# Performance work log

Measured on AMD Instinct MI355X. Metric: run time of the kernel, lower is better.

## Reference

```python
import jax, jax.numpy as jnp
import numpy as np

N_NODES = 50000
N_EDGES = 800000


def _sage_mean(x, src, dst, w, W_self, W_neigh, b, n_nodes):
    # DGL SAGEConv('mean') with edge_weight: messages m_e = w_e * h[src_e],
    # h_neigh[v] = sum_{e->v} m_e / in_degree(v)  (zero if no in-edges),
    # out = h @ W_self + h_neigh @ W_neigh + b
    msg = x[src] * w[:, None]                                   # [E, d]
    s = jax.ops.segment_sum(msg, dst, num_segments=n_nodes)     # [N, d]
    deg = jax.ops.segment_sum(jnp.ones_like(w), dst, num_segments=n_nodes)
    h_neigh = s / jnp.clip(deg, 1.0)[:, None]
    return x @ W_self + h_neigh @ W_neigh + b


def setup_inputs() -> dict:
    key = jax.random.key(0)
    ks = jax.random.split(key, 12)
    d_in, d_h = 64, 256
    inp = {
        'features': jax.random.normal(ks[0], (N_NODES, d_in), dtype=jnp.float32),
        'edge_src': jax.random.randint(ks[1], (N_EDGES,), 0, N_NODES, dtype=jnp.int32),
        'edge_dst': jax.random.randint(ks[2], (N_EDGES,), 0, N_NODES, dtype=jnp.int32),
        'edge_weights': jax.random.uniform(ks[3], (N_EDGES,), dtype=jnp.float32),
        'W1_self': jax.random.normal(ks[4], (d_in, d_h), dtype=jnp.float32) * (1.0 / np.sqrt(d_in)),
        'W1_neigh': jax.random.normal(ks[5], (d_in, d_h), dtype=jnp.float32) * (1.0 / np.sqrt(d_in)),
        'b1': jnp.zeros((d_h,), dtype=jnp.float32),
        'W2_self': jax.random.normal(ks[6], (d_h, 128), dtype=jnp.float32) * (1.0 / np.sqrt(d_h)),
        'W2_neigh': jax.random.normal(ks[7], (d_h, 128), dtype=jnp.float32) * (1.0 / np.sqrt(d_h)),
        'b2': jnp.zeros((128,), dtype=jnp.float32),
        'Wl1': jax.random.normal(ks[8], (128, 64), dtype=jnp.float32) * (1.0 / np.sqrt(128)),
        'bl1': jnp.zeros((64,), dtype=jnp.float32),
        'Wl2': jax.random.normal(ks[9], (64, 32), dtype=jnp.float32) * (1.0 / np.sqrt(64)),
        'bl2': jnp.zeros((32,), dtype=jnp.float32),
        'Wl3': jax.random.normal(ks[10], (32, 10), dtype=jnp.float32) * (1.0 / np.sqrt(32)),
        'bl3': jnp.zeros((10,), dtype=jnp.float32),
    }
    return inp


def reference(features, edge_src, edge_dst, edge_weights,
              W1_self, W1_neigh, b1, W2_self, W2_neigh, b2,
              Wl1, bl1, Wl2, bl2, Wl3, bl3):
    n = features.shape[0]
    x = features.reshape(n, -1)  # flatten (already 2D)
    x = jax.nn.relu(_sage_mean(x, edge_src, edge_dst, edge_weights,
                               W1_self, W1_neigh, b1, n))
    # conv2 is applied twice on identical inputs in the original; results are equal
    embeddings = _sage_mean(x, edge_src, edge_dst, edge_weights,
                            W2_self, W2_neigh, b2, n)
    h = jax.nn.relu(embeddings @ Wl1 + bl1)
    h = jax.nn.relu(h @ Wl2 + bl2)
    out = h @ Wl3 + bl3
    return (out, embeddings)
```

## Files before the change

kernel.cpp:

```cpp
#include <hip/hip_runtime.h>
#include <hip/hip_bf16.h>

#define N_NODES 50000
#define N_EDGES 800000
#define MT_TILES 3125
#define PR_TILES 1563

#define NBLK_SORT 200
#define CHUNK_SORT 4000
#define NBKT 196

typedef __attribute__((ext_vector_type(8))) short frag_ab;
typedef __attribute__((ext_vector_type(4))) float frag_cd;

static __device__ __forceinline__ unsigned short f2b(float f) {
    union { float f; unsigned u; } v; v.f = f;
    unsigned r = v.u + 0x7fffu + ((v.u >> 16) & 1u);
    return (unsigned short)(r >> 16);
}
static __device__ __forceinline__ float b2f(unsigned short b) {
    union { float f; unsigned u; } v; v.u = ((unsigned)b) << 16;
    return v.f;
}
static __device__ __forceinline__ float blo(unsigned p) { return b2f((unsigned short)(p & 0xffffu)); }
static __device__ __forceinline__ float bhi(unsigned p) { return b2f((unsigned short)(p >> 16)); }

static __device__ __forceinline__ unsigned short packBK_elem(const float* __restrict__ Wa,
                                                             const float* __restrict__ Wb,
                                                             int Ka, int N, int idx) {
    int j = idx & 7;
    int lane = (idx >> 3) & 63;
    int rest = idx >> 9;
    int ntiles = N >> 4;
    int nt = rest % ntiles;
    int kt = rest / ntiles;
    int kk = kt * 32 + (lane >> 4) * 8 + j;
    int nn = nt * 16 + (lane & 15);
    float v = (kk < Ka) ? Wa[kk * N + nn] : Wb[(kk - Ka) * N + nn];
    return f2b(v);
}
static __device__ __forceinline__ unsigned short packBN_elem(const float* __restrict__ Wa,
                                                             const float* __restrict__ Wb,
                                                             int Na, int N, int idx) {
    int j = idx & 7;
    int lane = (idx >> 3) & 63;
    int rest = idx >> 9;
    int ntiles = N >> 4;
    int nt = rest % ntiles;
    int kt = rest / ntiles;
    int kk = kt * 32 + (lane >> 4) * 8 + j;
    int nn = nt * 16 + (lane & 15);
    float v = (nn < Na) ? Wa[kk * Na + nn] : Wb[kk * (N - Na) + (nn - Na)];
    return f2b(v);
}

#define PREP_S0 800000
#define PREP_S1 (PREP_S0 + 32768)
#define PREP_S2 (PREP_S1 + 65536)
#define PREP_S3 (PREP_S2 + 8192)
#define PREP_S4 (PREP_S3 + 2048)
#define PREP_BLKS 3549

__global__ __launch_bounds__(256) void prep_p1_kernel(const float4* __restrict__ x4,
                                                      ushort4* __restrict__ xb4,
                                                      const float* __restrict__ W1s,
                                                      const float* __restrict__ W1n,
                                                      const float* __restrict__ W2s,
                                                      const float* __restrict__ W2n,
                                                      const float* __restrict__ Wl1,
                                                      const float* __restrict__ Wl2,
                                                      unsigned short* __restrict__ B1p,
                                                      unsigned short* __restrict__ B2p,
                                                      unsigned short* __restrict__ Bl1p,
                                                      unsigned short* __restrict__ Bl2p,
                                                      const int* __restrict__ dst,
                                                      int* __restrict__ G) {
    __shared__ int h[256];
    int bid = blockIdx.x;
    int t = threadIdx.x;
    if (bid >= PREP_BLKS) {
        int blk = bid - PREP_BLKS;
        h[t] = 0;
        __syncthreads();
        int base = blk * CHUNK_SORT;
        for (int i = t; i < CHUNK_SORT; i += 256)
            atomicAdd(&h[dst[base + i] >> 8], 1);
        __syncthreads();
        G[blk * 256 + t] = h[t];
        return;
    }
    int idx = bid * 256 + t;
    if (idx < PREP_S0) {
        float4 v = x4[idx];
        ushort4 o;
        o.x = f2b(v.x); o.y = f2b(v.y); o.z = f2b(v.z); o.w = f2b(v.w);
        xb4[idx] = o;
    } else if (idx < PREP_S1) {
        int i = idx - PREP_S0;
        B1p[i] = packBK_elem(W1s, W1n, 64, 256, i);
    } else if (idx < PREP_S2) {
        int i = idx - PREP_S1;
        B2p[i] = packBN_elem(W2s, W2n, 128, 256, i);
    } else if (idx < PREP_S3) {
        int i = idx - PREP_S2;
        Bl1p[i] = packBK_elem(Wl1, Wl1, 128, 64, i);
    } else {
        int i = idx - PREP_S3;
        Bl2p[i] = packBK_elem(Wl2, Wl2, 64, 32, i);
    }
}


__global__ __launch_bounds__(256) void p2a_scan(int* __restrict__ G,
                                                int* __restrict__ colsum) {
    __shared__ int sc[256];
    int b = blockIdx.x;
    int t = threadIdx.x;
    int v = (t < NBLK_SORT) ? G[t * 256 + b] : 0;
    sc[t] = v;
    __syncthreads();
    for (int off = 1; off < 256; off <<= 1) {
        int add = (t >= off) ? sc[t - off] : 0;
        __syncthreads();
        sc[t] += add;
        __syncthreads();
    }
    if (t < NBLK_SORT) G[t * 256 + b] = sc[t] - v;
    if (t == 255) colsum[b] = sc[255];
}

__global__ __launch_bounds__(256) void p2b_scan(const int* __restrict__ colsum,
                                                int* __restrict__ bucket_off,
                                                int* __restrict__ row_off) {
    __shared__ int sc[256];
    int t = threadIdx.x;
    int v = colsum[t];
    sc[t] = v;
    __syncthreads();
    for (int off = 1; off < 256; off <<= 1) {
        int add = (t >= off) ? sc[t - off] : 0;
        __syncthreads();
        sc[t] += add;
        __syncthreads();
    }
    bucket_off[t] = sc[t] - v;
    if (t == 255) row_off[N_NODES] = sc[255];
}

__global__ __launch_bounds__(256) void p3_scatter(const int* __restrict__ src,
                                                  const int* __restrict__ dst,
                                                  const float* __restrict__ w,
                                                  const int* __restrict__ G,
                                                  const int* __restrict__ bucket_off,
                                                  int* __restrict__ bdst,
                                                  int2* __restrict__ bsedge) {
    __shared__ int cur[256];
    int t = threadIdx.x;
    cur[t] = G[blockIdx.x * 256 + t] + bucket_off[t];
    __syncthreads();
    int base = blockIdx.x * CHUNK_SORT;
    for (int i = t; i < CHUNK_SORT; i += 256) {
        int e = base + i;
        int d = dst[e];
        int pos = atomicAdd(&cur[d >> 8], 1);
        bdst[pos] = d;
        bsedge[pos] = make_int2(src[e], __float_as_int(w[e]));
    }
}

__global__ __launch_bounds__(256) void p4_sort(const int* __restrict__ bucket_off,
                                               const int* __restrict__ bdst,
                                               const int2* __restrict__ bsedge,
                                               int* __restrict__ row_off,
                                               float* __restrict__ inv_deg,
                                               int2* __restrict__ sedge) {
    __shared__ int lcnt[256];
    __shared__ int lcur[256];
    __shared__ int sc[256];
    int t = threadIdx.x;
    int b = blockIdx.x;
    int e0 = bucket_off[b], e1 = bucket_off[b + 1];
    int d0 = b << 8;
    lcnt[t] = 0;
    __syncthreads();
    for (int e = e0 + t; e < e1; e += 256)
        atomicAdd(&lcnt[bdst[e] - d0], 1);
    __syncthreads();
    int v = lcnt[t];
    sc[t] = v;
    __syncthreads();
    for (int off = 1; off < 256; off <<= 1) {
        int add = (t >= off) ? sc[t - off] : 0;
        __syncthreads();
        sc[t] += add;
        __syncthreads();
    }
    int loff = e0 + sc[t] - v;
    lcur[t] = loff;
    int d = d0 + t;
    if (d < N_NODES) {
        row_off[d] = loff;
        inv_deg[d] = 1.0f / (float)(v > 0 ? v : 1);
    }
    __syncthreads();
    for (int e = e0 + t; e < e1; e += 256) {
        int dd = bdst[e];
        int2 sv = bsedge[e];
        int pos = atomicAdd(&lcur[dd - d0], 1);
        sedge[pos] = sv;
    }
}


__global__ __launch_bounds__(256) void agg64_kernel(const uint2* __restrict__ xb2,
                                                    const int* __restrict__ row_off,
                                                    const int2* __restrict__ sedge,
                                                    const float* __restrict__ inv_deg,
                                                    uint2* __restrict__ hn1b2) {
    int tid = threadIdx.x;
    int lane = tid & 63;
    int qr = lane >> 4;
    int l15 = lane & 15;
    int n = blockIdx.x * 4 + (tid >> 6);
    if (n >= N_NODES) return;
    int e0 = row_off[n], e1 = row_off[n + 1];
    float a0 = 0.f, a1 = 0.f, a2 = 0.f, a3 = 0.f;
    int e = e0;
    for (; e + 16 <= e1; e += 16) {
        int2 m0 = sedge[e + qr];
        int2 m1 = sedge[e + 4 + qr];
        int2 m2 = sedge[e + 8 + qr];
        int2 m3 = sedge[e + 12 + qr];
        uint2 p0 = xb2[m0.x * 16 + l15];
        uint2 p1 = xb2[m1.x * 16 + l15];
        uint2 p2 = xb2[m2.x * 16 + l15];
        uint2 p3 = xb2[m3.x * 16 + l15];
        float w0 = __int_as_float(m0.y), w1 = __int_as_float(m1.y);
        float w2 = __int_as_float(m2.y), w3 = __int_as_float(m3.y);
        a0 += w0 * blo(p0.x) + w1 * blo(p1.x) + w2 * blo(p2.x) + w3 * blo(p3.x);
        a1 += w0 * bhi(p0.x) + w1 * bhi(p1.x) + w2 * bhi(p2.x) + w3 * bhi(p3.x);
        a2 += w0 * blo(p0.y) + w1 * blo(p1.y) + w2 * blo(p2.y) + w3 * blo(p3.y);
        a3 += w0 * bhi(p0.y) + w1 * bhi(p1.y) + w2 * bhi(p2.y) + w3 * bhi(p3.y);
    }
    for (; e < e1; e += 4) {
        int ee = e + qr;
        if (ee < e1) {
            int2 m = sedge[ee];
            uint2 p = xb2[m.x * 16 + l15];
            float w = __int_as_float(m.y);
            a0 += w * blo(p.x); a1 += w * bhi(p.x);
            a2 += w * blo(p.y); a3 += w * bhi(p.y);
        }
    }
    a0 += __shfl_xor(a0, 16, 64); a1 += __shfl_xor(a1, 16, 64);
    a2 += __shfl_xor(a2, 16, 64); a3 += __shfl_xor(a3, 16, 64);
    a0 += __shfl_xor(a0, 32, 64); a1 += __shfl_xor(a1, 32, 64);
    a2 += __shfl_xor(a2, 32, 64); a3 += __shfl_xor(a3, 32, 64);
    if (qr == 0) {
        float id = inv_deg[n];
        uint2 o;
        o.x = (unsigned)f2b(a0 * id) | ((unsigned)f2b(a1 * id) << 16);
        o.y = (unsigned)f2b(a2 * id) | ((unsigned)f2b(a3 * id) << 16);
        hn1b2[n * 16 + l15] = o;
    }
}

__global__ __launch_bounds__(256) void agg128_kernel(const uint2* __restrict__ zb2,
                                                     const int* __restrict__ row_off,
                                                     const int2* __restrict__ sedge,
                                                     const float* __restrict__ inv_deg,
                                                     float* __restrict__ emb,
                                                     uint2* __restrict__ embb2) {
    int tid = threadIdx.x;
    int lane = tid & 63;
    int hf = lane >> 5;
    int l31 = lane & 31;
    int n = blockIdx.x * 4 + (tid >> 6);
    if (n >= N_NODES) return;
    int e0 = row_off[n], e1 = row_off[n + 1];
    float a0 = 0.f, a1 = 0.f, a2 = 0.f, a3 = 0.f;
    int e = e0;
    for (; e + 16 <= e1; e += 16) {
        int2 m0 = sedge[e + hf];
        int2 m1 = sedge[e + 2 + hf];
        int2 m2 = sedge[e + 4 + hf];
        int2 m3 = sedge[e + 6 + hf];
        int2 m4 = sedge[e + 8 + hf];
        int2 m5 = sedge[e + 10 + hf];
        int2 m6 = sedge[e + 12 + hf];
        int2 m7 = sedge[e + 14 + hf];
        uint2 p0 = zb2[m0.x * 32 + l31];
        uint2 p1 = zb2[m1.x * 32 + l31];
        uint2 p2 = zb2[m2.x * 32 + l31];
        uint2 p3 = zb2[m3.x * 32 + l31];
        uint2 p4 = zb2[m4.x * 32 + l31];
        uint2 p5 = zb2[m5.x * 32 + l31];
        uint2 p6 = zb2[m6.x * 32 + l31];
        uint2 p7 = zb2[m7.x * 32 + l31];
        float w0 = __int_as_float(m0.y), w1 = __int_as_float(m1.y);
        float w2 = __int_as_float(m2.y), w3 = __int_as_float(m3.y);
        float w4 = __int_as_float(m4.y), w5 = __int_as_float(m5.y);
        float w6 = __int_as_float(m6.y), w7 = __int_as_float(m7.y);
        a0 += w0 * blo(p0.x) + w1 * blo(p1.x) + w2 * blo(p2.x) + w3 * blo(p3.x)
            + w4 * blo(p4.x) + w5 * blo(p5.x) + w6 * blo(p6.x) + w7 * blo(p7.x);
        a1 += w0 * bhi(p0.x) + w1 * bhi(p1.x) + w2 * bhi(p2.x) + w3 * bhi(p3.x)
            + w4 * bhi(p4.x) + w5 * bhi(p5.x) + w6 * bhi(p6.x) + w7 * bhi(p7.x);
        a2 += w0 * blo(p0.y) + w1 * blo(p1.y) + w2 * blo(p2.y) + w3 * blo(p3.y)
            + w4 * blo(p4.y) + w5 * blo(p5.y) + w6 * blo(p6.y) + w7 * blo(p7.y);
        a3 += w0 * bhi(p0.y) + w1 * bhi(p1.y) + w2 * bhi(p2.y) + w3 * bhi(p3.y)
            + w4 * bhi(p4.y) + w5 * bhi(p5.y) + w6 * bhi(p6.y) + w7 * bhi(p7.y);
    }
    for (; e < e1; e += 2) {
        int ee = e + hf;
        if (ee < e1) {
            int2 m = sedge[ee];
            uint2 p = zb2[m.x * 32 + l31];
            float w = __int_as_float(m.y);
            a0 += w * blo(p.x); a1 += w * bhi(p.x);
            a2 += w * blo(p.y); a3 += w * bhi(p.y);
        }
    }
    a0 += __shfl_xor(a0, 32, 64); a1 += __shfl_xor(a1, 32, 64);
    a2 += __shfl_xor(a2, 32, 64); a3 += __shfl_xor(a3, 32, 64);
    if (hf == 0) {
        float id = inv_deg[n];
        float4 self = ((const float4*)emb)[n * 32 + l31];
        float v0 = self.x + a0 * id;
        float v1 = self.y + a1 * id;
        float v2 = self.z + a2 * id;
        float v3 = self.w + a3 * id;
        ((float4*)emb)[n * 32 + l31] = make_float4(v0, v1, v2, v3);
        uint2 o;
        o.x = (unsigned)f2b(v0) | ((unsigned)f2b(v1) << 16);
        o.y = (unsigned)f2b(v2) | ((unsigned)f2b(v3) << 16);
        embb2[n * 32 + l31] = o;
    }
}


__global__ __launch_bounds__(256) void gemm1_mfma(const unsigned short* __restrict__ xb,
                                                  const unsigned short* __restrict__ hn1b,
                                                  const unsigned short* __restrict__ Bp,
                                                  const float* __restrict__ b1,
                                                  unsigned short* __restrict__ x1b) {
    __shared__ __align__(16) unsigned short sB[8192];
    int tid = threadIdx.x;
    int lane = tid & 63;
    int wv = tid >> 6;
    int mt = blockIdx.x * 4 + wv;
    if (mt >= MT_TILES) mt = MT_TILES - 1;
    int q = lane >> 4;
    int rl = lane & 15;
    int row = mt * 16 + rl;
    frag_ab a[4];
    a[0] = *(const frag_ab*)(xb + row * 64 + q * 8);
    a[1] = *(const frag_ab*)(xb + row * 64 + q * 8 + 32);
    a[2] = *(const frag_ab*)(hn1b + row * 64 + q * 8);
    a[3] = *(const frag_ab*)(hn1b + row * 64 + q * 8 + 32);
    frag_cd acc[16];
    #pragma unroll
    for (int nt = 0; nt < 16; nt++) acc[nt] = (frag_cd){0.f, 0.f, 0.f, 0.f};
    #pragma unroll
    for (int kt = 0; kt < 4; kt++) {
        __syncthreads();
        #pragma unroll
        for (int i = 0; i < 4; i++) {
            int idx = i * 256 + tid;
            ((float4*)sB)[idx] = ((const float4*)(Bp + kt * 8192))[idx];
        }
        __syncthreads();
        #pragma unroll
        for (int nt = 0; nt < 16; nt++) {
            frag_ab b = *(const frag_ab*)(sB + (nt * 64 + lane) * 8);
            acc[nt] = __builtin_amdgcn_mfma_f32_16x16x32_bf16(a[kt], b, acc[nt], 0, 0, 0);
        }
    }
    int r0 = mt * 16;
    #pragma unroll
    for (int nt = 0; nt < 16; nt++) {
        int c = nt * 16 + rl;
        float bias = b1[c];
        #pragma unroll
        for (int i = 0; i < 4; i++) {
            int r = r0 + q * 4 + i;
            float v = acc[nt][i] + bias;
            v = v > 0.f ? v : 0.f;
            x1b[r * 256 + c] = f2b(v);
        }
    }
}

__global__ __launch_bounds__(256) void gemm2_mfma(const unsigned short* __restrict__ x1b,
                                                  const unsigned short* __restrict__ Bp,
                                                  const float* __restrict__ b2,
                                                  float* __restrict__ emb,
                                                  unsigned short* __restrict__ zb) {
    __shared__ __align__(16) unsigned short sB[8192];
    int tid = threadIdx.x;
    int lane = tid & 63;
    int wv = tid >> 6;
    int mt = blockIdx.x * 4 + wv;
    if (mt >= MT_TILES) mt = MT_TILES - 1;
    int q = lane >> 4;
    int rl = lane & 15;
    int row = mt * 16 + rl;
    const unsigned short* arow = x1b + row * 256 + q * 8;
    frag_ab a[8];
    #pragma unroll
    for (int kt = 0; kt < 8; kt++) a[kt] = *(const frag_ab*)(arow + kt * 32);
    frag_cd acc[16];
    #pragma unroll
    for (int nt = 0; nt < 16; nt++) acc[nt] = (frag_cd){0.f, 0.f, 0.f, 0.f};
    #pragma unroll
    for (int kt = 0; kt < 8; kt++) {
        __syncthreads();
        #pragma unroll
        for (int i = 0; i < 4; i++) {
            int idx = i * 256 + tid;
            ((float4*)sB)[idx] = ((const float4*)(Bp + kt * 8192))[idx];
        }
        __syncthreads();
        #pragma unroll
        for (int nt = 0; nt < 16; nt++) {
            frag_ab b = *(const frag_ab*)(sB + (nt * 64 + lane) * 8);
            acc[nt] = __builtin_amdgcn_mfma_f32_16x16x32_bf16(a[kt], b, acc[nt], 0, 0, 0);
        }
    }
    int r0 = mt * 16;
    #pragma unroll
    for (int nt = 0; nt < 8; nt++) {
        int c = nt * 16 + rl;
        float bias = b2[c];
        #pragma unroll
        for (int i = 0; i < 4; i++) {
            int r = r0 + q * 4 + i;
            emb[r * 128 + c] = acc[nt][i] + bias;
        }
    }
    #pragma unroll
    for (int nt = 8; nt < 16; nt++) {
        int c = (nt - 8) * 16 + rl;
        #pragma unroll
        for (int i = 0; i < 4; i++) {
            int r = r0 + q * 4 + i;
            zb[r * 128 + c] = f2b(acc[nt][i]);
        }
    }
}

__global__ __launch_bounds__(256) void mlp1_mfma(const unsigned short* __restrict__ embb,
                                                 const unsigned short* __restrict__ Bp,
                                                 const float* __restrict__ bl1,
                                                 unsigned short* __restrict__ h64b) {
    int tid = threadIdx.x;
    int lane = tid & 63;
    int wv = tid >> 6;
    int pr = blockIdx.x * 4 + wv;
    if (pr >= PR_TILES) pr = PR_TILES - 1;
    int mt0 = pr * 2;
    int mt1 = mt0 + 1; if (mt1 >= MT_TILES) mt1 = MT_TILES - 1;
    int q = lane >> 4;
    int rl = lane & 15;
    const unsigned short* a0row = embb + (mt0 * 16 + rl) * 128 + q * 8;
    const unsigned short* a1row = embb + (mt1 * 16 + rl) * 128 + q * 8;
    const frag_ab* bp = (const frag_ab*)Bp;
    frag_cd acc0[4], acc1[4];
    #pragma unroll
    for (int nt = 0; nt < 4; nt++) {
        acc0[nt] = (frag_cd){0.f, 0.f, 0.f, 0.f};
        acc1[nt] = (frag_cd){0.f, 0.f, 0.f, 0.f};
    }
    #pragma unroll
    for (int kt = 0; kt < 4; kt++) {
        frag_ab a0 = *(const frag_ab*)(a0row + kt * 32);
        frag_ab a1 = *(const frag_ab*)(a1row + kt * 32);
        #pragma unroll
        for (int nt = 0; nt < 4; nt++) {
            frag_ab b = bp[(kt * 4 + nt) * 64 + lane];
            acc0[nt] = __builtin_amdgcn_mfma_f32_16x16x32_bf16(a0, b, acc0[nt], 0, 0, 0);
            acc1[nt] = __builtin_amdgcn_mfma_f32_16x16x32_bf16(a1, b, acc1[nt], 0, 0, 0);
        }
    }
    int r0a = mt0 * 16 + q * 4, r0b = mt1 * 16 + q * 4;
    #pragma unroll
    for (int nt = 0; nt < 4; nt++) {
        int c = nt * 16 + rl;
        float bias = bl1[c];
        #pragma unroll
        for (int i = 0; i < 4; i++) {
            float v0 = acc0[nt][i] + bias;
            float v1 = acc1[nt][i] + bias;
            h64b[(r0a + i) * 64 + c] = f2b(v0 > 0.f ? v0 : 0.f);
            h64b[(r0b + i) * 64 + c] = f2b(v1 > 0.f ? v1 : 0.f);
        }
    }
}

__global__ __launch_bounds__(256) void mlp23_mfma(const unsigned short* __restrict__ h64b,
                                                  const unsigned short* __restrict__ Bp,
                                                  const float* __restrict__ bl2,
                                                  const float* __restrict__ Wl3,
                                                  const float* __restrict__ bl3,
                                                  float* __restrict__ out) {
    __shared__ float hs[64][33];
    int tid = threadIdx.x;
    int lane = tid & 63;
    int wv = tid >> 6;
    int mt = blockIdx.x * 4 + wv;
    if (mt >= MT_TILES) mt = MT_TILES - 1;
    int q = lane >> 4;
    int rl = lane & 15;
    const unsigned short* arow = h64b + (mt * 16 + rl) * 64 + q * 8;
    const frag_ab* bp = (const frag_ab*)Bp;
    frag_cd acc[2];
    #pragma unroll
    for (int nt = 0; nt < 2; nt++) acc[nt] = (frag_cd){0.f, 0.f, 0.f, 0.f};
    #pragma unroll
    for (int kt = 0; kt < 2; kt++) {
        frag_ab a = *(const frag_ab*)(arow + kt * 32);
        #pragma unroll
        for (int nt = 0; nt < 2; nt++) {
            frag_ab b = bp[(kt * 2 + nt) * 64 + lane];
            acc[nt] = __builtin_amdgcn_mfma_f32_16x16x32_bf16(a, b, acc[nt], 0, 0, 0);
        }
    }
    #pragma unroll
    for (int nt = 0; nt < 2; nt++) {
        int c = nt * 16 + rl;
        float bias = bl2[c];
        #pragma unroll
        for (int i = 0; i < 4; i++) {
            int lr = wv * 16 + q * 4 + i;
            float v = acc[nt][i] + bias;
            hs[lr][c] = v > 0.f ? v : 0.f;
        }
    }
    __syncthreads();
    int base = blockIdx.x * 64;
    for (int idx = tid; idx < 640; idx += 256) {
        int lr = idx / 10;
        int j = idx - lr * 10;
        int n = base + lr;
        if (n < N_NODES) {
            float a = bl3[j];
            #pragma unroll
            for (int k = 0; k < 32; k++) a += hs[lr][k] * Wl3[k * 10 + j];
            out[n * 10 + j] = a;
        }
    }
}


extern "C" void kernel_launch(void* const* d_in, const int* in_sizes, int n_in,
                              void* d_out, int out_size, void* d_ws, size_t ws_size,
                              hipStream_t stream) {
    const float* x   = (const float*)d_in[0];
    const int* esrc  = (const int*)d_in[1];
    const int* edst  = (const int*)d_in[2];
    const float* ew  = (const float*)d_in[3];
    const float* W1s = (const float*)d_in[4];
    const float* W1n = (const float*)d_in[5];
    const float* b1  = (const float*)d_in[6];
    const float* W2s = (const float*)d_in[7];
    const float* W2n = (const float*)d_in[8];
    const float* b2  = (const float*)d_in[9];
    const float* Wl1 = (const float*)d_in[10];
    const float* bl1 = (const float*)d_in[11];
    const float* Wl2 = (const float*)d_in[12];
    const float* bl2 = (const float*)d_in[13];
    const float* Wl3 = (const float*)d_in[14];
    const float* bl3 = (const float*)d_in[15];

    float* out = (float*)d_out;
    float* emb = out + 500000;

    char* ws = (char*)d_ws;
    size_t off = 0;
    auto alloc = [&](size_t bytes) -> void* {
        void* p = ws + off;
        off = (off + bytes + 255) & ~(size_t)255;
        return p;
    };
    int*   row_off = (int*)alloc((size_t)(N_NODES + 1) * 4);
    float* inv_deg = (float*)alloc((size_t)N_NODES * 4);
    int*   G       = (int*)alloc((size_t)NBLK_SORT * 256 * 4);
    int*   colsum  = (int*)alloc(256 * 4);
    int*   bkt_off = (int*)alloc(257 * 4);
    int*   bdst    = (int*)alloc((size_t)N_EDGES * 4);
    int2*  bsedge  = (int2*)alloc((size_t)N_EDGES * 8);
    int2*  sedge   = (int2*)alloc((size_t)N_EDGES * 8);
    unsigned short* xb   = (unsigned short*)alloc((size_t)N_NODES * 64 * 2);
    unsigned short* hn1b = (unsigned short*)alloc((size_t)N_NODES * 64 * 2);
    unsigned short* x1b  = (unsigned short*)alloc((size_t)N_NODES * 256 * 2);
    unsigned short* zb   = (unsigned short*)alloc((size_t)N_NODES * 128 * 2);
    unsigned short* embb = (unsigned short*)alloc((size_t)N_NODES * 128 * 2);
    unsigned short* h64b = (unsigned short*)alloc((size_t)N_NODES * 64 * 2);
    unsigned short* B1p  = (unsigned short*)alloc(128 * 256 * 2);
    unsigned short* B2p  = (unsigned short*)alloc(256 * 256 * 2);
    unsigned short* Bl1p = (unsigned short*)alloc(128 * 64 * 2);
    unsigned short* Bl2p = (unsigned short*)alloc(64 * 32 * 2);

    prep_p1_kernel<<<PREP_BLKS + NBLK_SORT, 256, 0, stream>>>(
        (const float4*)x, (ushort4*)xb, W1s, W1n, W2s, W2n, Wl1, Wl2,
        B1p, B2p, Bl1p, Bl2p, edst, G);

    p2a_scan<<<256, 256, 0, stream>>>(G, colsum);
    p2b_scan<<<1, 256, 0, stream>>>(colsum, bkt_off, row_off);
    p3_scatter<<<NBLK_SORT, 256, 0, stream>>>(esrc, edst, ew, G, bkt_off, bdst, bsedge);
    p4_sort<<<NBKT, 256, 0, stream>>>(bkt_off, bdst, bsedge, row_off, inv_deg, sedge);

    const int PBLK = (PR_TILES + 3) / 4;
    const int GBLK = (MT_TILES + 3) / 4;
    const int ABLK = (N_NODES + 3) / 4;

    agg64_kernel<<<ABLK, 256, 0, stream>>>((const uint2*)xb, row_off, sedge,
                                           inv_deg, (uint2*)hn1b);
    gemm1_mfma<<<GBLK, 256, 0, stream>>>(xb, hn1b, B1p, b1, x1b);

    gemm2_mfma<<<GBLK, 256, 0, stream>>>(x1b, B2p, b2, emb, zb);
    agg128_kernel<<<ABLK, 256, 0, stream>>>((const uint2*)zb, row_off, sedge,
                                            inv_deg, emb, (uint2*)embb);

    mlp1_mfma<<<PBLK, 256, 0, stream>>>(embb, Bl1p, bl1, h64b);
    mlp23_mfma<<<GBLK, 256, 0, stream>>>(h64b, Bl2p, bl2, Wl3, bl3, out);
}
```

Baseline: 279.9 us.

## Split aggregation kernels into feature slices and store self term as bf16

Both aggregation kernels now launch several grids of node groups, each block handling one 32-feature slice. Each lane gathers one 32-bit bf16 pair per edge instead of 8 bytes, so the gathered feature working set per pass is smaller and should cache better. gemm2 now writes its self-projection plus bias in bf16 into a combined 256-wide buffer rather than an fp32 emb array. agg128 reads that self term and writes the final fp32 emb and its bf16 copy. The cost is reading the edge lists and row offsets several times over, and rounding the self term to bf16 before it reaches the embeddings.

```diff
diff --git a/kernel.cpp b/kernel.cpp
--- a/kernel.cpp
+++ b/kernel.cpp
@@ -9,6 +9,7 @@
 #define NBLK_SORT 200
 #define CHUNK_SORT 4000
 #define NBKT 196
+#define AGG_G 12500
 
 typedef __attribute__((ext_vector_type(8))) short frag_ab;
 typedef __attribute__((ext_vector_type(4))) float frag_cd;
@@ -212,128 +213,131 @@
 }
 
 
-__global__ __launch_bounds__(256) void agg64_kernel(const uint2* __restrict__ xb2,
+__global__ __launch_bounds__(256) void agg64_kernel(const unsigned* __restrict__ xb32,
                                                     const int* __restrict__ row_off,
                                                     const int2* __restrict__ sedge,
                                                     const float* __restrict__ inv_deg,
-                                                    uint2* __restrict__ hn1b2) {
+                                                    unsigned* __restrict__ hn1b32) {
+    int bi = blockIdx.x;
+    int s = bi / AGG_G;
+    int g = bi - s * AGG_G;
     int tid = threadIdx.x;
     int lane = tid & 63;
     int qr = lane >> 4;
     int l15 = lane & 15;
-    int n = blockIdx.x * 4 + (tid >> 6);
-    if (n >= N_NODES) return;
+    int n = g * 4 + (tid >> 6);
+    int xoff = s * 16 + l15;
     int e0 = row_off[n], e1 = row_off[n + 1];
-    float a0 = 0.f, a1 = 0.f, a2 = 0.f, a3 = 0.f;
+    float a0 = 0.f, a1 = 0.f;
     int e = e0;
-    for (; e + 16 <= e1; e += 16) {
+    for (; e + 32 <= e1; e += 32) {
         int2 m0 = sedge[e + qr];
         int2 m1 = sedge[e + 4 + qr];
         int2 m2 = sedge[e + 8 + qr];
         int2 m3 = sedge[e + 12 + qr];
-        uint2 p0 = xb2[m0.x * 16 + l15];
-        uint2 p1 = xb2[m1.x * 16 + l15];
-        uint2 p2 = xb2[m2.x * 16 + l15];
-        uint2 p3 = xb2[m3.x * 16 + l15];
+        int2 m4 = sedge[e + 16 + qr];
+        int2 m5 = sedge[e + 20 + qr];
+        int2 m6 = sedge[e + 24 + qr];
+        int2 m7 = sedge[e + 28 + qr];
+        unsigned p0 = xb32[m0.x * 32 + xoff];
+        unsigned p1 = xb32[m1.x * 32 + xoff];
+        unsigned p2 = xb32[m2.x * 32 + xoff];
+        unsigned p3 = xb32[m3.x * 32 + xoff];
+        unsigned p4 = xb32[m4.x * 32 + xoff];
+        unsigned p5 = xb32[m5.x * 32 + xoff];
+        unsigned p6 = xb32[m6.x * 32 + xoff];
+        unsigned p7 = xb32[m7.x * 32 + xoff];
         float w0 = __int_as_float(m0.y), w1 = __int_as_float(m1.y);
         float w2 = __int_as_float(m2.y), w3 = __int_as_float(m3.y);
-        a0 += w0 * blo(p0.x) + w1 * blo(p1.x) + w2 * blo(p2.x) + w3 * blo(p3.x);
-        a1 += w0 * bhi(p0.x) + w1 * bhi(p1.x) + w2 * bhi(p2.x) + w3 * bhi(p3.x);
-        a2 += w0 * blo(p0.y) + w1 * blo(p1.y) + w2 * blo(p2.y) + w3 * blo(p3.y);
-        a3 += w0 * bhi(p0.y) + w1 * bhi(p1.y) + w2 * bhi(p2.y) + w3 * bhi(p3.y);
+        float w4 = __int_as_float(m4.y), w5 = __int_as_float(m5.y);
+        float w6 = __int_as_float(m6.y), w7 = __int_as_float(m7.y);
+        a0 += w0 * blo(p0) + w1 * blo(p1) + w2 * blo(p2) + w3 * blo(p3)
+            + w4 * blo(p4) + w5 * blo(p5) + w6 * blo(p6) + w7 * blo(p7);
+        a1 += w0 * bhi(p0) + w1 * bhi(p1) + w2 * bhi(p2) + w3 * bhi(p3)
+            + w4 * bhi(p4) + w5 * bhi(p5) + w6 * bhi(p6) + w7 * bhi(p7);
     }
     for (; e < e1; e += 4) {
         int ee = e + qr;
         if (ee < e1) {
             int2 m = sedge[ee];
-            uint2 p = xb2[m.x * 16 + l15];
+            unsigned p = xb32[m.x * 32 + xoff];
             float w = __int_as_float(m.y);
-            a0 += w * blo(p.x); a1 += w * bhi(p.x);
-            a2 += w * blo(p.y); a3 += w * bhi(p.y);
+            a0 += w * blo(p);
+            a1 += w * bhi(p);
         }
     }
     a0 += __shfl_xor(a0, 16, 64); a1 += __shfl_xor(a1, 16, 64);
-    a2 += __shfl_xor(a2, 16, 64); a3 += __shfl_xor(a3, 16, 64);
     a0 += __shfl_xor(a0, 32, 64); a1 += __shfl_xor(a1, 32, 64);
-    a2 += __shfl_xor(a2, 32, 64); a3 += __shfl_xor(a3, 32, 64);
     if (qr == 0) {
         float id = inv_deg[n];
-        uint2 o;
-        o.x = (unsigned)f2b(a0 * id) | ((unsigned)f2b(a1 * id) << 16);
-        o.y = (unsigned)f2b(a2 * id) | ((unsigned)f2b(a3 * id) << 16);
-        hn1b2[n * 16 + l15] = o;
-    }
-}
-
-__global__ __launch_bounds__(256) void agg128_kernel(const uint2* __restrict__ zb2,
+        hn1b32[n * 32 + xoff] = (unsigned)f2b(a0 * id) | ((unsigned)f2b(a1 * id) << 16);
+    }
+}
+
+__global__ __launch_bounds__(256) void agg128_kernel(const unsigned* __restrict__ sz32,
                                                      const int* __restrict__ row_off,
                                                      const int2* __restrict__ sedge,
                                                      const float* __restrict__ inv_deg,
                                                      float* __restrict__ emb,
-                                                     uint2* __restrict__ embb2) {
+                                                     unsigned* __restrict__ embb32) {
+    int bi = blockIdx.x;
+    int s = bi / AGG_G;
+    int g = bi - s * AGG_G;
     int tid = threadIdx.x;
     int lane = tid & 63;
-    int hf = lane >> 5;
-    int l31 = lane & 31;
-    int n = blockIdx.x * 4 + (tid >> 6);
-    if (n >= N_NODES) return;
+    int qr = lane >> 4;
+    int l15 = lane & 15;
+    int n = g * 4 + (tid >> 6);
+    int soff = s * 16 + l15;
+    int zoff = 64 + soff;
     int e0 = row_off[n], e1 = row_off[n + 1];
-    float a0 = 0.f, a1 = 0.f, a2 = 0.f, a3 = 0.f;
+    float a0 = 0.f, a1 = 0.f;
     int e = e0;
-    for (; e + 16 <= e1; e += 16) {
-        int2 m0 = sedge[e + hf];
-        int2 m1 = sedge[e + 2 + hf];
-        int2 m2 = sedge[e + 4 + hf];
-        int2 m3 = sedge[e + 6 + hf];
-        int2 m4 = sedge[e + 8 + hf];
-        int2 m5 = sedge[e + 10 + hf];
-        int2 m6 = sedge[e + 12 + hf];
-        int2 m7 = sedge[e + 14 + hf];
-        uint2 p0 = zb2[m0.x * 32 + l31];
-        uint2 p1 = zb2[m1.x * 32 + l31];
-        uint2 p2 = zb2[m2.x * 32 + l31];
-        uint2 p3 = zb2[m3.x * 32 + l31];
-        uint2 p4 = zb2[m4.x * 32 + l31];
-        uint2 p5 = zb2[m5.x * 32 + l31];
-        uint2 p6 = zb2[m6.x * 32 + l31];
-        uint2 p7 = zb2[m7.x * 32 + l31];
+    for (; e + 32 <= e1; e += 32) {
+        int2 m0 = sedge[e + qr];
+        int2 m1 = sedge[e + 4 + qr];
+        int2 m2 = sedge[e + 8 + qr];
+        int2 m3 = sedge[e + 12 + qr];
+        int2 m4 = sedge[e + 16 + qr];
+        int2 m5 = sedge[e + 20 + qr];
+        int2 m6 = sedge[e + 24 + qr];
+        int2 m7 = sedge[e + 28 + qr];
+        unsigned p0 = sz32[m0.x * 128 + zoff];
+        unsigned p1 = sz32[m1.x * 128 + zoff];
+        unsigned p2 = sz32[m2.x * 128 + zoff];
+        unsigned p3 = sz32[m3.x * 128 + zoff];
+        unsigned p4 = sz32[m4.x * 128 + zoff];
+        unsigned p5 = sz32[m5.x * 128 + zoff];
+        unsigned p6 = sz32[m6.x * 128 + zoff];
+        unsigned p7 = sz32[m7.x * 128 + zoff];
         float w0 = __int_as_float(m0.y), w1 = __int_as_float(m1.y);
         float w2 = __int_as_float(m2.y), w3 = __int_as_float(m3.y);
         float w4 = __int_as_float(m4.y), w5 = __int_as_float(m5.y);
         float w6 = __int_as_float(m6.y), w7 = __int_as_float(m7.y);
-        a0 += w0 * blo(p0.x) + w1 * blo(p1.x) + w2 * blo(p2.x) + w3 * blo(p3.x)
-            + w4 * blo(p4.x) + w5 * blo(p5.x) + w6 * blo(p6.x) + w7 * blo(p7.x);
-        a1 += w0 * bhi(p0.x) + w1 * bhi(p1.x) + w2 * bhi(p2.x) + w3 * bhi(p3.x)
-            + w4 * bhi(p4.x) + w5 * bhi(p5.x) + w6 * bhi(p6.x) + w7 * bhi(p7.x);
-        a2 += w0 * blo(p0.y) + w1 * blo(p1.y) + w2 * blo(p2.y) + w3 * blo(p3.y)
-            + w4 * blo(p4.y) + w5 * blo(p5.y) + w6 * blo(p6.y) + w7 * blo(p7.y);
-        a3 += w0 * bhi(p0.y) + w1 * bhi(p1.y) + w2 * bhi(p2.y) + w3 * bhi(p3.y)
-            + w4 * bhi(p4.y) + w5 * bhi(p5.y) + w6 * bhi(p6.y) + w7 * bhi(p7.y);
-    }
-    for (; e < e1; e += 2) {
-        int ee = e + hf;
+        a0 += w0 * blo(p0) + w1 * blo(p1) + w2 * blo(p2) + w3 * blo(p3)
+            + w4 * blo(p4) + w5 * blo(p5) + w6 * blo(p6) + w7 * blo(p7);
+        a1 += w0 * bhi(p0) + w1 * bhi(p1) + w2 * bhi(p2) + w3 * bhi(p3)
+            + w4 * bhi(p4) + w5 * bhi(p5) + w6 * bhi(p6) + w7 * bhi(p7);
+    }
+    for (; e < e1; e += 4) {
+        int ee = e + qr;
         if (ee < e1) {
             int2 m = sedge[ee];
-            uint2 p = zb2[m.x * 32 + l31];
+            unsigned p = sz32[m.x * 128 + zoff];
             float w = __int_as_float(m.y);
-            a0 += w * blo(p.x); a1 += w * bhi(p.x);
-            a2 += w * blo(p.y); a3 += w * bhi(p.y);
-        }
-    }
+            a0 += w * blo(p);
+            a1 += w * bhi(p);
+        }
+    }
+    a0 += __shfl_xor(a0, 16, 64); a1 += __shfl_xor(a1, 16, 64);
     a0 += __shfl_xor(a0, 32, 64); a1 += __shfl_xor(a1, 32, 64);
-    a2 += __shfl_xor(a2, 32, 64); a3 += __shfl_xor(a3, 32, 64);
-    if (hf == 0) {
+    if (qr == 0) {
         float id = inv_deg[n];
-        float4 self = ((const float4*)emb)[n * 32 + l31];
-        float v0 = self.x + a0 * id;
-        float v1 = self.y + a1 * id;
-        float v2 = self.z + a2 * id;
-        float v3 = self.w + a3 * id;
-        ((float4*)emb)[n * 32 + l31] = make_float4(v0, v1, v2, v3);
-        uint2 o;
-        o.x = (unsigned)f2b(v0) | ((unsigned)f2b(v1) << 16);
-        o.y = (unsigned)f2b(v2) | ((unsigned)f2b(v3) << 16);
-        embb2[n * 32 + l31] = o;
+        unsigned sp = sz32[n * 128 + soff];
+        float vx = blo(sp) + a0 * id;
+        float vy = bhi(sp) + a1 * id;
+        ((float2*)emb)[n * 64 + soff] = make_float2(vx, vy);
+        embb32[n * 64 + soff] = (unsigned)f2b(vx) | ((unsigned)f2b(vy) << 16);
     }
 }
 
@@ -393,8 +397,7 @@
 __global__ __launch_bounds__(256) void gemm2_mfma(const unsigned short* __restrict__ x1b,
                                                   const unsigned short* __restrict__ Bp,
                                                   const float* __restrict__ b2,
-                                                  float* __restrict__ emb,
-                                                  unsigned short* __restrict__ zb) {
+                                                  unsigned short* __restrict__ sz) {
     __shared__ __align__(16) unsigned short sB[8192];
     int tid = threadIdx.x;
     int lane = tid & 63;
@@ -428,22 +431,13 @@
     }
     int r0 = mt * 16;
     #pragma unroll
-    for (int nt = 0; nt < 8; nt++) {
+    for (int nt = 0; nt < 16; nt++) {
         int c = nt * 16 + rl;
-        float bias = b2[c];
+        float bias = (nt < 8) ? b2[c] : 0.f;
         #pragma unroll
         for (int i = 0; i < 4; i++) {
             int r = r0 + q * 4 + i;
-            emb[r * 128 + c] = acc[nt][i] + bias;
-        }
-    }
-    #pragma unroll
-    for (int nt = 8; nt < 16; nt++) {
-        int c = (nt - 8) * 16 + rl;
-        #pragma unroll
-        for (int i = 0; i < 4; i++) {
-            int r = r0 + q * 4 + i;
-            zb[r * 128 + c] = f2b(acc[nt][i]);
+            sz[r * 256 + c] = f2b(acc[nt][i] + bias);
         }
     }
 }
@@ -592,7 +586,7 @@
     unsigned short* xb   = (unsigned short*)alloc((size_t)N_NODES * 64 * 2);
     unsigned short* hn1b = (unsigned short*)alloc((size_t)N_NODES * 64 * 2);
     unsigned short* x1b  = (unsigned short*)alloc((size_t)N_NODES * 256 * 2);
-    unsigned short* zb   = (unsigned short*)alloc((size_t)N_NODES * 128 * 2);
+    unsigned short* sz   = (unsigned short*)alloc((size_t)N_NODES * 256 * 2);
     unsigned short* embb = (unsigned short*)alloc((size_t)N_NODES * 128 * 2);
     unsigned short* h64b = (unsigned short*)alloc((size_t)N_NODES * 64 * 2);
     unsigned short* B1p  = (unsigned short*)alloc(128 * 256 * 2);
@@ -611,15 +605,14 @@
 
     const int PBLK = (PR_TILES + 3) / 4;
     const int GBLK = (MT_TILES + 3) / 4;
-    const int ABLK = (N_NODES + 3) / 4;
-
-    agg64_kernel<<<ABLK, 256, 0, stream>>>((const uint2*)xb, row_off, sedge,
-                                           inv_deg, (uint2*)hn1b);
+
+    agg64_kernel<<<2 * AGG_G, 256, 0, stream>>>((const unsigned*)xb, row_off, sedge,
+                                                inv_deg, (unsigned*)hn1b);
     gemm1_mfma<<<GBLK, 256, 0, stream>>>(xb, hn1b, B1p, b1, x1b);
 
-    gemm2_mfma<<<GBLK, 256, 0, stream>>>(x1b, B2p, b2, emb, zb);
-    agg128_kernel<<<ABLK, 256, 0, stream>>>((const uint2*)zb, row_off, sedge,
-                                            inv_deg, emb, (uint2*)embb);
+    gemm2_mfma<<<GBLK, 256, 0, stream>>>(x1b, B2p, b2, sz);
+    agg128_kernel<<<4 * AGG_G, 256, 0, stream>>>((const unsigned*)sz, row_off, sedge,
+                                                 inv_deg, emb, (unsigned*)embb);
 
     mlp1_mfma<<<PBLK, 256, 0, stream>>>(embb, Bl1p, bl1, h64b);
     mlp23_mfma<<<GBLK, 256, 0, stream>>>(h64b, Bl2p, bl2, Wl3, bl3, out);
```

Measured after the change: 371.2 us. +32.6%, slower.
